# Optimization experiments

Hardware: AMD Instinct MI355X
Metric: run time of the kernel (lower is better)

Reference implementation:

```python
import jax, jax.numpy as jnp
import numpy as np

B, S, DM, NH, WIN = 2, 2048, 1024, 16, 256
DH = DM // NH          # 64
DFF = 4 * DM           # 4096
WIDTHS = (256, 512, 1024)  # 1024 == hidden -> identity (no adapter in torch ModuleDict)


def _ln(x, g, b, eps=1e-5):
    m = jnp.mean(x, -1, keepdims=True)
    v = jnp.var(x, -1, keepdims=True)
    return (x - m) * jax.lax.rsqrt(v + eps) * g + b


def _gelu(t):
    return jax.nn.gelu(t, approximate=False)  # torch nn.GELU default = exact erf


def setup_inputs() -> dict:
    key = jax.random.key(0)
    ks = iter(jax.random.split(key, 32))

    def lin(fi, fo):
        # xavier_uniform(gain=1/sqrt(2)) ~ scale sqrt(2/(fi+fo))/sqrt(2); normal init is fine for a numeric reference
        std = float((1.0 / np.sqrt(2.0)) * np.sqrt(2.0 / (fi + fo)))
        return (jax.random.normal(next(ks), (fi, fo), jnp.float32) * std,
                jnp.zeros((fo,), jnp.float32))

    inp = {}
    inp['x'] = jax.random.normal(next(ks), (B, S, DM), jnp.float32)
    inp['width_multiplier'] = jax.random.uniform(next(ks), (B, S, 1), jnp.float32)
    # attention projections
    inp['wq'], inp['bq'] = lin(DM, DM)
    inp['wk'], inp['bk'] = lin(DM, DM)
    inp['wv'], inp['bv'] = lin(DM, DM)
    inp['wo'], inp['bo'] = lin(DM, DM)
    inp['lnq_g'] = jnp.ones((DH,), jnp.float32); inp['lnq_b'] = jnp.zeros((DH,), jnp.float32)
    inp['lnk_g'] = jnp.ones((DH,), jnp.float32); inp['lnk_b'] = jnp.zeros((DH,), jnp.float32)
    # base FFN
    inp['fc1_w'], inp['fc1_b'] = lin(DM, DFF)
    inp['fc2_w'], inp['fc2_b'] = lin(DFF, DM)
    inp['lni_g'] = jnp.ones((DM,), jnp.float32); inp['lni_b'] = jnp.zeros((DM,), jnp.float32)
    inp['lnh_g'] = jnp.ones((DFF,), jnp.float32); inp['lnh_b'] = jnp.zeros((DFF,), jnp.float32)
    # width adapters (for widths != hidden_dim)
    inp['a256_w1'], inp['a256_b1'] = lin(DM, 256)
    inp['a256_w2'], inp['a256_b2'] = lin(256, DM)
    inp['a512_w1'], inp['a512_b1'] = lin(DM, 512)
    inp['a512_w2'], inp['a512_b2'] = lin(512, DM)
    # router output: index into WIDTHS per token
    inp['width_idx'] = jax.random.randint(next(ks), (B, S), 0, 3)
    return inp


def reference(x, width_multiplier, wq, bq, wk, bk, wv, bv, wo, bo,
              lnq_g, lnq_b, lnk_g, lnk_b, fc1_w, fc1_b, fc2_w, fc2_b,
              lni_g, lni_b, lnh_g, lnh_b,
              a256_w1, a256_b1, a256_w2, a256_b2,
              a512_w1, a512_b1, a512_w2, a512_b2, width_idx):
    # ---- local causal windowed attention pathway ----
    q = (x @ wq + bq).reshape(B, S, NH, DH)
    k = (x @ wk + bk).reshape(B, S, NH, DH)
    v = (x @ wv + bv).reshape(B, S, NH, DH)
    q = _ln(q, lnq_g, lnq_b)  # per-head-dim LayerNorm (torch ln_q on [B,S,H,Dh])
    k = _ln(k, lnk_g, lnk_b)
    scores = jnp.einsum('bihd,bjhd->bhij', q, k) / np.float32(np.sqrt(DH))
    ii = jnp.arange(S)[:, None]
    jj = jnp.arange(S)[None, :]
    allowed = (jj <= ii) & (ii - jj <= WIN)  # causal + local window
    scores = jnp.where(allowed[None, None], scores, -jnp.inf)
    probs = jax.nn.softmax(scores, axis=-1)
    attn = jnp.einsum('bhij,bjhd->bihd', probs, v).reshape(B, S, DM)
    h = x + attn @ wo + bo  # residual around attention pathway

    # ---- width-adaptive FFN ----
    xn = _ln(h, lni_g, lni_b)
    hid = _ln(_gelu(xn @ fc1_w + fc1_b), lnh_g, lnh_b)
    base = hid @ fc2_w + fc2_b
    # per-width adapters, combined by routing mask (dense compute, masked scatter)
    a0 = _gelu(xn @ a256_w1 + a256_b1) @ a256_w2 + a256_b2
    a1 = _gelu(xn @ a512_w1 + a512_b1) @ a512_w2 + a512_b2
    a2 = xn  # width == hidden_dim -> identity pass-through
    m0 = (width_idx == 0)[..., None]
    m1 = (width_idx == 1)[..., None]
    m2 = (width_idx == 2)[..., None]
    adaptive = jnp.where(m0, a0, 0.0) + jnp.where(m1, a1, 0.0) + jnp.where(m2, a2, 0.0)
    ffn_out = base * width_multiplier + adaptive * (1.0 - width_multiplier)
    return h + ffn_out
```

## Files before the change

### kernel.cpp

```cpp
#include <hip/hip_runtime.h>
#include <math.h>

#define B_   2
#define S_   2048
#define DM_  1024
#define NH_  16
#define DH_  64
#define DFF_ 4096
#define WIN_ 256
#define MTOK (B_*S_)

typedef unsigned short ushort_t;
typedef short s16x8 __attribute__((ext_vector_type(8)));
typedef float f32x4 __attribute__((ext_vector_type(4)));

__device__ __forceinline__ float b2f(ushort_t u) {
    union { unsigned int i; float f; } c; c.i = ((unsigned int)u) << 16; return c.f;
}
__device__ __forceinline__ ushort_t f2b(float f) {
    union { float f; unsigned int i; } c; c.f = f;
    unsigned int r = c.i + 0x7fffu + ((c.i >> 16) & 1u);
    return (ushort_t)(r >> 16);
}
__device__ __forceinline__ float gelu_fast(float x) {
    const float u = 0.7978845608f * x * fmaf(0.044715f, x * x, 1.0f);
    const float e = __expf(2.0f * u);
    const float t = 1.0f - 2.0f / (e + 1.0f);
    return 0.5f * x * (1.0f + t);
}
__device__ __forceinline__ void gload16(const void* g, void* l) {
    __builtin_amdgcn_global_load_lds(
        (const __attribute__((address_space(1))) unsigned int*)g,
        (__attribute__((address_space(3))) unsigned int*)l, 16, 0, 0);
}
__device__ __forceinline__ int xcd_swz(int wgid, int nwg) {
    const int nx = 8;
    const int q = nwg / nx, r = nwg % nx;
    const int xcd = wgid % nx, lo = wgid / nx;
    const int base = (xcd < r) ? xcd * (q + 1) : r * (q + 1) + (xcd - r) * q;
    return base + lo;
}

__device__ __forceinline__ void gemm_loop(
    const ushort_t* __restrict__ A, int lda,
    const ushort_t* __restrict__ Bt, int ldb,
    int Kc, int bx, int by, f32x4 (&acc)[4][4])
{
    __shared__ __align__(16) ushort_t As[256 * 64];
    __shared__ __align__(16) ushort_t Bs[128 * 64];

    const int tid  = threadIdx.x;
    const int lane = tid & 63;
    const int w    = tid >> 6;
    const int row0 = by * 256;
    const int col0 = bx * 128;

    const int srow = lane >> 3;
    const int sk   = (lane & 7) * 8;
    const int wr   = (w >> 1) * 64;
    const int wc   = (w & 1) * 64;
    const int lr   = lane & 15;
    const int lk   = (lane >> 4) * 8;

    for (int k0 = 0; k0 < Kc; k0 += 64) {
        #pragma unroll
        for (int i = 0; i < 4; ++i) {
            const int c = i * 8 + w;
            const int cr = c * 8 + srow;
            gload16(A + (size_t)(row0 + cr) * lda + k0 + sk, (char*)As + c * 1024);
        }
        #pragma unroll
        for (int i = 0; i < 2; ++i) {
            const int c = i * 8 + w;
            const int cr = c * 8 + srow;
            gload16(Bt + (size_t)(col0 + cr) * ldb + k0 + sk, (char*)Bs + c * 1024);
        }
        __syncthreads();
        #pragma unroll
        for (int ks = 0; ks < 2; ++ks) {
            s16x8 af[4], bfr[4];
            #pragma unroll
            for (int mi = 0; mi < 4; ++mi)
                af[mi] = *(const s16x8*)&As[(wr + mi * 16 + lr) * 64 + ks * 32 + lk];
            #pragma unroll
            for (int ni = 0; ni < 4; ++ni)
                bfr[ni] = *(const s16x8*)&Bs[(wc + ni * 16 + lr) * 64 + ks * 32 + lk];
            #pragma unroll
            for (int mi = 0; mi < 4; ++mi)
                #pragma unroll
                for (int ni = 0; ni < 4; ++ni)
                    acc[mi][ni] = __builtin_amdgcn_mfma_f32_16x16x32_bf16(
                        af[mi], bfr[ni], acc[mi][ni], 0, 0, 0);
        }
        __syncthreads();
    }
}

__global__ __launch_bounds__(512) void gemm_qkvln(
    const ushort_t* __restrict__ A, const ushort_t* __restrict__ Bt,
    const float* __restrict__ bias,
    const float* __restrict__ qg, const float* __restrict__ qb,
    const float* __restrict__ kg, const float* __restrict__ kb,
    ushort_t* __restrict__ qh, ushort_t* __restrict__ kh, ushort_t* __restrict__ vh)
{
    f32x4 acc[4][4] = {};
    gemm_loop(A, 1024, Bt, 1024, 1024, blockIdx.x, blockIdx.y, acc);

    const int lane = threadIdx.x & 63;
    const int w    = threadIdx.x >> 6;
    const int wr   = (w >> 1) * 64;
    const int wc   = (w & 1) * 64;
    const int row0 = blockIdx.y * 256;
    const int col0 = blockIdx.x * 128;
    const int crow = (lane >> 4) * 4;
    const int ccol = lane & 15;
    const int sel  = (col0 + wc) >> 10;
    const int hh   = ((col0 + wc) & 1023) >> 6;
    ushort_t* dst = (sel == 0) ? qh : (sel == 1) ? kh : vh;

    #pragma unroll
    for (int mi = 0; mi < 4; ++mi) {
        float val[4][4];
        float s1[4] = {}, sq[4] = {};
        #pragma unroll
        for (int ni = 0; ni < 4; ++ni) {
            const float bc = bias[col0 + wc + ni * 16 + ccol];
            #pragma unroll
            for (int r = 0; r < 4; ++r) {
                const float v = acc[mi][ni][r] + bc;
                val[ni][r] = v;
                s1[r] += v;
                sq[r] = fmaf(v, v, sq[r]);
            }
        }
        if (sel < 2) {
            #pragma unroll
            for (int r = 0; r < 4; ++r) {
                #pragma unroll
                for (int m = 1; m < 16; m <<= 1) {
                    s1[r] += __shfl_xor(s1[r], m);
                    sq[r] += __shfl_xor(sq[r], m);
                }
            }
        }
        #pragma unroll
        for (int r = 0; r < 4; ++r) {
            const int r_abs = row0 + wr + mi * 16 + crow + r;
            const int bb = r_abs >> 11, ss = r_abs & 2047;
            const size_t db = (((size_t)(bb * NH_ + hh)) * S_ + ss) * 64;
            const float mean = s1[r] * 0.015625f;
            const float var  = sq[r] * 0.015625f - mean * mean;
            const float rstd = rsqrtf(var + 1e-5f);
            #pragma unroll
            for (int ni = 0; ni < 4; ++ni) {
                const int d = ni * 16 + ccol;
                float v = val[ni][r];
                if (sel == 0)      v = ((v - mean) * rstd * qg[d] + qb[d]) * 0.125f;
                else if (sel == 1) v = (v - mean) * rstd * kg[d] + kb[d];
                dst[db + d] = f2b(v);
            }
        }
    }
}

__global__ __launch_bounds__(512) void gemm_fc1ad(
    const ushort_t* __restrict__ A, const ushort_t* __restrict__ Bt,
    const float* __restrict__ bias,
    ushort_t* __restrict__ hid, ushort_t* __restrict__ tA)
{
    f32x4 acc[4][4] = {};
    gemm_loop(A, 1024, Bt, 1024, 1024, blockIdx.x, blockIdx.y, acc);

    const int lane = threadIdx.x & 63;
    const int w    = threadIdx.x >> 6;
    const int wr   = (w >> 1) * 64;
    const int wc   = (w & 1) * 64;
    const int row0 = blockIdx.y * 256;
    const int col0 = blockIdx.x * 128;
    const int crow = (lane >> 4) * 4;
    const int ccol = lane & 15;
    const bool isad = (col0 >= 4096);
    ushort_t* D = isad ? tA : hid;
    const int stride = isad ? 768 : 4096;
    const int cb     = isad ? 4096 : 0;

    #pragma unroll
    for (int ni = 0; ni < 4; ++ni) {
        const int col = col0 + wc + ni * 16 + ccol;
        const float bc = bias[col];
        #pragma unroll
        for (int mi = 0; mi < 4; ++mi) {
            #pragma unroll
            for (int r = 0; r < 4; ++r) {
                const int row = row0 + wr + mi * 16 + crow + r;
                D[(size_t)row * stride + (col - cb)] = f2b(gelu_fast(acc[mi][ni][r] + bc));
            }
        }
    }
}

__device__ __forceinline__ void epi_raw(
    f32x4 (&acc)[4][4], float* __restrict__ C, int N, int bx, int by)
{
    const int lane = threadIdx.x & 63;
    const int w    = threadIdx.x >> 6;
    const int wr   = (w >> 1) * 64;
    const int wc   = (w & 1) * 64;
    const int crow = (lane >> 4) * 4;
    const int ccol = lane & 15;
    #pragma unroll
    for (int ni = 0; ni < 4; ++ni) {
        const int col = bx * 128 + wc + ni * 16 + ccol;
        #pragma unroll
        for (int mi = 0; mi < 4; ++mi) {
            #pragma unroll
            for (int r = 0; r < 4; ++r) {
                const int row = by * 256 + wr + mi * 16 + crow + r;
                C[(size_t)row * N + col] = acc[mi][ni][r];
            }
        }
    }
}

__global__ __launch_bounds__(512) void gemm_wo_sk(
    const ushort_t* __restrict__ A, const ushort_t* __restrict__ Wt,
    float* __restrict__ p0, float* __restrict__ p1)
{
    const int z = blockIdx.z;
    f32x4 acc[4][4] = {};
    gemm_loop(A + z * 512, 1024, Wt + z * 512, 1024, 512, blockIdx.x, blockIdx.y, acc);
    epi_raw(acc, z ? p1 : p0, 1024, blockIdx.x, blockIdx.y);
}

__global__ __launch_bounds__(512) void gemm_fc2_sk(
    const ushort_t* __restrict__ A, const ushort_t* __restrict__ Bt,
    float* __restrict__ p0, float* __restrict__ p1)
{
    const int z = blockIdx.z;
    f32x4 acc[4][4] = {};
    gemm_loop(A + z * 2048, 4096, Bt + z * 2048, 4096, 2048, blockIdx.x, blockIdx.y, acc);
    epi_raw(acc, z ? p1 : p0, 1024, blockIdx.x, blockIdx.y);
}

__global__ __launch_bounds__(512) void gemm_adapters(
    const ushort_t* __restrict__ tA, const ushort_t* __restrict__ w2a,
    const ushort_t* __restrict__ w2b, const float* __restrict__ b2a,
    const float* __restrict__ b2b, float* __restrict__ a0, float* __restrict__ a1)
{
    const int z = blockIdx.z;
    const ushort_t* Ap = z ? tA + 256 : tA;
    const ushort_t* Wp = z ? w2b : w2a;
    const float*    bp = z ? b2b : b2a;
    float*          Cp = z ? a1 : a0;
    const int Kz = z ? 512 : 256;
    f32x4 acc[4][4] = {};
    gemm_loop(Ap, 768, Wp, Kz, Kz, blockIdx.x, blockIdx.y, acc);

    const int lane = threadIdx.x & 63;
    const int w    = threadIdx.x >> 6;
    const int wr   = (w >> 1) * 64;
    const int wc   = (w & 1) * 64;
    const int crow = (lane >> 4) * 4;
    const int ccol = lane & 15;
    #pragma unroll
    for (int ni = 0; ni < 4; ++ni) {
        const int col = blockIdx.x * 128 + wc + ni * 16 + ccol;
        const float bc = bp[col];
        #pragma unroll
        for (int mi = 0; mi < 4; ++mi) {
            #pragma unroll
            for (int r = 0; r < 4; ++r) {
                const int row = blockIdx.y * 256 + wr + mi * 16 + crow + r;
                Cp[(size_t)row * 1024 + col] = acc[mi][ni][r] + bc;
            }
        }
    }
}

__device__ __forceinline__ void wtrans_core(
    const float* __restrict__ W, ushort_t* __restrict__ Wt, int K, int N,
    int bx, int by)
{
    __shared__ float tile[32][33];
    const int n0 = bx * 32, k0 = by * 32;
    const int tx = threadIdx.x & 31, ty = threadIdx.x >> 5;
    #pragma unroll
    for (int j = 0; j < 4; ++j)
        tile[ty + j * 8][tx] = W[(size_t)(k0 + ty + j * 8) * N + n0 + tx];
    __syncthreads();
    #pragma unroll
    for (int j = 0; j < 4; ++j)
        Wt[(size_t)(n0 + ty + j * 8) * K + k0 + tx] = f2b(tile[tx][ty + j * 8]);
}

__global__ __launch_bounds__(256) void wtrans(
    const float* __restrict__ W, ushort_t* __restrict__ Wt, int K, int N)
{
    wtrans_core(W, Wt, K, N, blockIdx.x, blockIdx.y);
}

__global__ __launch_bounds__(256) void wtrans4(
    const float* w0, const float* w1, const float* w2, const float* w3,
    ushort_t* d0, ushort_t* d1, ushort_t* d2, ushort_t* d3)
{
    const int z = blockIdx.z;
    const float* W = (z == 0) ? w0 : (z == 1) ? w1 : (z == 2) ? w2 : w3;
    ushort_t* Wt   = (z == 0) ? d0 : (z == 1) ? d1 : (z == 2) ? d2 : d3;
    wtrans_core(W, Wt, 1024, 1024, blockIdx.x, blockIdx.y);
}

__global__ __launch_bounds__(256) void conv_f2b(
    const float* __restrict__ in, ushort_t* __restrict__ out, int n4)
{
    const int i = blockIdx.x * 256 + threadIdx.x;
    if (i >= n4) return;
    float4 v = ((const float4*)in)[i];
    ushort4 o; o.x = f2b(v.x); o.y = f2b(v.y); o.z = f2b(v.z); o.w = f2b(v.w);
    ((ushort4*)out)[i] = o;
}

__global__ __launch_bounds__(256) void prep_bias(
    const float* bq, const float* bk, const float* bv, const float* fb,
    const float* b1, const float* b2, float* bqkv, float* bfc1ad)
{
    const int t = blockIdx.x * 256 + threadIdx.x;
    if (t < 1024) { bqkv[t] = bq[t]; bqkv[1024 + t] = bk[t]; bqkv[2048 + t] = bv[t]; }
    if (t < 4096)      bfc1ad[t] = fb[t];
    else if (t < 4352) bfc1ad[t] = b1[t - 4096];
    else if (t < 4864) bfc1ad[t] = b2[t - 4352];
}

__global__ __launch_bounds__(256) void attn_mfma(
    const ushort_t* __restrict__ qh, const ushort_t* __restrict__ kh,
    const ushort_t* __restrict__ vh, ushort_t* __restrict__ o)
{
    __shared__ __align__(16) ushort_t Ks[64 * 64];
    __shared__ __align__(16) ushort_t Vt[64 * 64];
    __shared__ __align__(16) ushort_t Pl[4 * 16 * 64];

    const int bid = xcd_swz(blockIdx.x, gridDim.x);
    const int qt  = bid & 31;
    const int hh  = (bid >> 5) & 15;
    const int b   = bid >> 9;
    const int wq   = threadIdx.x >> 6;
    const int lane = threadIdx.x & 63;
    const int lg  = lane >> 4;
    const int lq  = lane & 15;

    const int i0  = qt * 64;
    const int iw0 = i0 + wq * 16;
    const int i_l = iw0 + lq;

    const size_t plane = ((size_t)(b * NH_ + hh)) * S_ * 64;

    s16x8 qf[2];
    {
        const ushort_t* qp = qh + plane + (size_t)(iw0 + lq) * 64 + lg * 8;
        qf[0] = *(const s16x8*)(qp);
        qf[1] = *(const s16x8*)(qp + 32);
    }

    f32x4 acc[4] = {};
    float M = -1e30f, L = 0.0f;

    const int jstart = (i0 - WIN_) > 0 ? (i0 - WIN_) : 0;
    const int nt     = (i0 + 64 - jstart) >> 6;

    const int srow0 = threadIdx.x >> 3;
    const int sd0   = (threadIdx.x & 7) * 8;

    for (int t = 0; t < nt; ++t) {
        const int j0 = jstart + t * 64;

        #pragma unroll
        for (int pass = 0; pass < 2; ++pass) {
            const int skey = srow0 + pass * 32;
            const size_t src = plane + (size_t)(j0 + skey) * 64 + sd0;
            s16x8 k8 = *(const s16x8*)(kh + src);
            s16x8 v8 = *(const s16x8*)(vh + src);
            *(s16x8*)&Ks[skey * 64 + (sd0 ^ ((skey & 7) << 3))] = k8;
            #pragma unroll
            for (int e = 0; e < 8; ++e) {
                const int d = sd0 + e;
                Vt[d * 64 + (skey ^ (((d >> 1) & 7) << 3))] = (ushort_t)v8[e];
            }
        }
        __syncthreads();

        f32x4 sc[4];
        #pragma unroll
        for (int kt = 0; kt < 4; ++kt) {
            const int krow = kt * 16 + lq;
            const int swk = (krow & 7) << 3;
            s16x8 k0 = *(const s16x8*)&Ks[krow * 64 + ((lg * 8) ^ swk)];
            s16x8 k1 = *(const s16x8*)&Ks[krow * 64 + ((lg * 8 + 32) ^ swk)];
            f32x4 z = {};
            z = __builtin_amdgcn_mfma_f32_16x16x32_bf16(k0, qf[0], z, 0, 0, 0);
            z = __builtin_amdgcn_mfma_f32_16x16x32_bf16(k1, qf[1], z, 0, 0, 0);
            sc[kt] = z;
        }

        const bool fullv = (j0 + 63 <= iw0) && (iw0 + 15 - j0 <= WIN_);
        if (!fullv) {
            #pragma unroll
            for (int kt = 0; kt < 4; ++kt)
                #pragma unroll
                for (int r = 0; r < 4; ++r) {
                    const int jv = j0 + kt * 16 + lg * 4 + r;
                    const int dd = i_l - jv;
                    const bool ok = (dd >= 0) && (dd <= WIN_);
                    sc[kt][r] = ok ? sc[kt][r] : -1e30f;
                }
        }
        float mx = -1e30f;
        #pragma unroll
        for (int kt = 0; kt < 4; ++kt)
            #pragma unroll
            for (int r = 0; r < 4; ++r) mx = fmaxf(mx, sc[kt][r]);
        mx = fmaxf(mx, __shfl_xor(mx, 16));
        mx = fmaxf(mx, __shfl_xor(mx, 32));
        const float nM = fmaxf(M, mx);
        const float alpha = __expf(M - nM);
        M = nM;
        float ts = 0.0f;
        float ev[16];
        #pragma unroll
        for (int kt = 0; kt < 4; ++kt)
            #pragma unroll
            for (int r = 0; r < 4; ++r) {
                float e = __expf(sc[kt][r] - nM);
                if (!fullv) e = (sc[kt][r] > -1e29f) ? e : 0.0f;
                ev[kt * 4 + r] = e;
                ts += e;
            }
        ts += __shfl_xor(ts, 16);
        ts += __shfl_xor(ts, 32);
        L = L * alpha + ts;

        {
            ushort_t* pw = Pl + wq * 1024;
            const int swq = (lq & 7) << 3;
            #pragma unroll
            for (int kt = 0; kt < 4; ++kt)
                #pragma unroll
                for (int pr = 0; pr < 2; ++pr) {
                    const int key0 = kt * 16 + lg * 4 + pr * 2;
                    const unsigned int pk =
                        (unsigned int)f2b(ev[kt * 4 + pr * 2]) |
                        ((unsigned int)f2b(ev[kt * 4 + pr * 2 + 1]) << 16);
                    *(unsigned int*)&pw[lq * 64 + (key0 ^ swq)] = pk;
                }
        }

        float ar[4];
        #pragma unroll
        for (int r = 0; r < 4; ++r) ar[r] = __shfl(alpha, lg * 4 + r);
        #pragma unroll
        for (int dt = 0; dt < 4; ++dt)
            #pragma unroll
            for (int r = 0; r < 4; ++r) acc[dt][r] *= ar[r];

        {
            const ushort_t* pw = Pl + wq * 1024;
            const int swq = (lq & 7) << 3;
            s16x8 pf0 = *(const s16x8*)&pw[lq * 64 + ((lg * 8) ^ swq)];
            s16x8 pf1 = *(const s16x8*)&pw[lq * 64 + ((lg * 8 + 32) ^ swq)];
            #pragma unroll
            for (int dt = 0; dt < 4; ++dt) {
                const int d = dt * 16 + lq;
                const int swd = ((d >> 1) & 7) << 3;
                s16x8 v0 = *(const s16x8*)&Vt[d * 64 + ((lg * 8) ^ swd)];
                s16x8 v1 = *(const s16x8*)&Vt[d * 64 + ((lg * 8 + 32) ^ swd)];
                acc[dt] = __builtin_amdgcn_mfma_f32_16x16x32_bf16(pf0, v0, acc[dt], 0, 0, 0);
                acc[dt] = __builtin_amdgcn_mfma_f32_16x16x32_bf16(pf1, v1, acc[dt], 0, 0, 0);
            }
        }
        __syncthreads();
    }

    const float inv = 1.0f / L;
    float ir[4];
    #pragma unroll
    for (int r = 0; r < 4; ++r) ir[r] = __shfl(inv, lg * 4 + r);
    #pragma unroll
    for (int dt = 0; dt < 4; ++dt)
        #pragma unroll
        for (int r = 0; r < 4; ++r) {
            const int qq = lg * 4 + r;
            o[((size_t)(b * S_ + iw0 + qq)) * DM_ + hh * 64 + dt * 16 + lq] =
                f2b(acc[dt][r] * ir[r]);
        }
}

__global__ __launch_bounds__(256) void ln_token_h(
    const float* __restrict__ p0, const float* __restrict__ p1,
    const float* __restrict__ bo, const float* __restrict__ x,
    float* __restrict__ hb, ushort_t* __restrict__ xnb,
    const float* __restrict__ g, const float* __restrict__ b)
{
    const int t = blockIdx.x;
    const size_t base = (size_t)t * 1024;
    float vals[4];
    float s = 0.0f, s2 = 0.0f;
    #pragma unroll
    for (int i = 0; i < 4; ++i) {
        const int idx = i * 256 + threadIdx.x;
        const float v = x[base + idx] + p0[base + idx] + p1[base + idx] + bo[idx];
        hb[base + idx] = v;
        vals[i] = v;
        s += v;
        s2 = fmaf(v, v, s2);
    }
    #pragma unroll
    for (int o = 32; o >= 1; o >>= 1) { s += __shfl_xor(s, o); s2 += __shfl_xor(s2, o); }
    __shared__ float rs[4], rq[4];
    const int wid = threadIdx.x >> 6, lane = threadIdx.x & 63;
    if (lane == 0) { rs[wid] = s; rq[wid] = s2; }
    __syncthreads();
    s  = rs[0] + rs[1] + rs[2] + rs[3];
    s2 = rq[0] + rq[1] + rq[2] + rq[3];
    const float mean = s * (1.0f / 1024.0f);
    const float var  = s2 * (1.0f / 1024.0f) - mean * mean;
    const float rstd = rsqrtf(var + 1e-5f);
    #pragma unroll
    for (int i = 0; i < 4; ++i) {
        const int idx = i * 256 + threadIdx.x;
        xnb[base + idx] = f2b((vals[i] - mean) * rstd * g[idx] + b[idx]);
    }
}

template <int N>
__global__ __launch_bounds__(256) void ln_token2(
    const ushort_t* __restrict__ in, ushort_t* __restrict__ outp,
    const float* __restrict__ g, const float* __restrict__ b)
{
    constexpr int NPT = N / 256;
    const int t = blockIdx.x;
    const ushort_t* row = in + (size_t)t * N;
    float vals[NPT];
    float s = 0.0f, s2 = 0.0f;
    #pragma unroll
    for (int i = 0; i < NPT; ++i) {
        float x = b2f(row[i * 256 + threadIdx.x]);
        vals[i] = x;
        s += x;
        s2 = fmaf(x, x, s2);
    }
    #pragma unroll
    for (int o = 32; o >= 1; o >>= 1) { s += __shfl_xor(s, o); s2 += __shfl_xor(s2, o); }
    __shared__ float rs[4], rq[4];
    const int wid = threadIdx.x >> 6, lane = threadIdx.x & 63;
    if (lane == 0) { rs[wid] = s; rq[wid] = s2; }
    __syncthreads();
    s  = rs[0] + rs[1] + rs[2] + rs[3];
    s2 = rq[0] + rq[1] + rq[2] + rq[3];
    const float mean = s * (1.0f / N);
    const float var  = s2 * (1.0f / N) - mean * mean;
    const float rstd = rsqrtf(var + 1e-5f);
    #pragma unroll
    for (int i = 0; i < NPT; ++i) {
        const int idx = i * 256 + threadIdx.x;
        outp[(size_t)t * N + idx] = f2b((vals[i] - mean) * rstd * g[idx] + b[idx]);
    }
}

__global__ __launch_bounds__(256) void combine3(
    float* __restrict__ outp, const float* __restrict__ p1,
    const float* __restrict__ fc2b, const float* __restrict__ h,
    const ushort_t* __restrict__ xnb, const float* __restrict__ a0,
    const float* __restrict__ a1, const float* __restrict__ wm,
    const int* __restrict__ widx)
{
    const size_t idx = (size_t)blockIdx.x * 256 + threadIdx.x;
    const int t   = (int)(idx >> 10);
    const int col = (int)(idx & 1023);
    const float w = wm[t];
    const int sel = widx[t];
    const float base = outp[idx] + p1[idx] + fc2b[col];
    const float ad = (sel == 0) ? a0[idx] : ((sel == 1) ? a1[idx] : b2f(xnb[idx]));
    outp[idx] = h[idx] + base * w + ad * (1.0f - w);
}

extern "C" void kernel_launch(void* const* d_in, const int* in_sizes, int n_in,
                              void* d_out, int out_size, void* d_ws, size_t ws_size,
                              hipStream_t stream)
{
    const float* x     = (const float*)d_in[0];
    const float* wm    = (const float*)d_in[1];
    const float* wq    = (const float*)d_in[2];
    const float* bq    = (const float*)d_in[3];
    const float* wk    = (const float*)d_in[4];
    const float* bk    = (const float*)d_in[5];
    const float* wv    = (const float*)d_in[6];
    const float* bv    = (const float*)d_in[7];
    const float* wo    = (const float*)d_in[8];
    const float* bo    = (const float*)d_in[9];
    const float* lnq_g = (const float*)d_in[10];
    const float* lnq_b = (const float*)d_in[11];
    const float* lnk_g = (const float*)d_in[12];
    const float* lnk_b = (const float*)d_in[13];
    const float* fc1_w = (const float*)d_in[14];
    const float* fc1_b = (const float*)d_in[15];
    const float* fc2_w = (const float*)d_in[16];
    const float* fc2_b = (const float*)d_in[17];
    const float* lni_g = (const float*)d_in[18];
    const float* lni_b = (const float*)d_in[19];
    const float* lnh_g = (const float*)d_in[20];
    const float* lnh_b = (const float*)d_in[21];
    const float* a256_w1 = (const float*)d_in[22];
    const float* a256_b1 = (const float*)d_in[23];
    const float* a256_w2 = (const float*)d_in[24];
    const float* a256_b2 = (const float*)d_in[25];
    const float* a512_w1 = (const float*)d_in[26];
    const float* a512_b1 = (const float*)d_in[27];
    const float* a512_w2 = (const float*)d_in[28];
    const float* a512_b2 = (const float*)d_in[29];
    const int*   widx    = (const int*)d_in[30];

    float* out = (float*)d_out;

    char* p = (char*)d_ws;
    auto alloc = [&](size_t bytes) { char* r = p; p += (bytes + 255) & ~(size_t)255; return r; };
    float*    ascr  = (float*)   alloc((size_t)MTOK * 2048 * 4);
    float*    hb    = (float*)   alloc((size_t)MTOK * 1024 * 4);
    ushort_t* xnb   = (ushort_t*)alloc((size_t)MTOK * 1024 * 2);
    ushort_t* hidb  = (ushort_t*)alloc((size_t)MTOK * 4096 * 2);
    ushort_t* tA    = (ushort_t*)alloc((size_t)MTOK * 768 * 2);
    ushort_t* WqkvT = (ushort_t*)alloc((size_t)3072 * 1024 * 2);
    ushort_t* WoT   = (ushort_t*)alloc((size_t)1024 * 1024 * 2);
    ushort_t* fc1adT= (ushort_t*)alloc((size_t)4864 * 1024 * 2);
    ushort_t* fc2T  = (ushort_t*)alloc((size_t)1024 * 4096 * 2);
    ushort_t* w2aT  = (ushort_t*)alloc((size_t)1024 * 256 * 2);
    ushort_t* w2bT  = (ushort_t*)alloc((size_t)1024 * 512 * 2);
    float*    bqkv  = (float*)   alloc(3072 * 4);
    float*    bfc1ad= (float*)   alloc(4864 * 4);
    float*    p1    = (float*)   alloc((size_t)MTOK * 1024 * 4);
    ushort_t* xb    = hidb;
    ushort_t* attnb = hidb + (size_t)MTOK * 1024;
    ushort_t* qh    = hidb + (size_t)MTOK * 2048;
    ushort_t* kh    = hidb + (size_t)MTOK * 3072;
    ushort_t* vh    = (ushort_t*)p1;
    float*    a0    = ascr;
    float*    a1    = ascr + (size_t)MTOK * 1024;

    const dim3 blk(256);
    const dim3 blk512(512);

    prep_bias<<<20, blk, 0, stream>>>(bq, bk, bv, fc1_b, a256_b1, a512_b1,
                                      bqkv, bfc1ad);
    conv_f2b<<<(MTOK * 1024 / 4 + 255) / 256, blk, 0, stream>>>(x, xb, MTOK * 1024 / 4);
    wtrans4<<<dim3(32, 32, 4), blk, 0, stream>>>(wq, wk, wv, wo,
        WqkvT, WqkvT + 1024 * 1024, WqkvT + 2048 * 1024, WoT);
    wtrans<<<dim3(128, 32), blk, 0, stream>>>(fc1_w, fc1adT, 1024, 4096);
    wtrans<<<dim3(8, 32),   blk, 0, stream>>>(a256_w1, fc1adT + (size_t)4096 * 1024, 1024, 256);
    wtrans<<<dim3(16, 32),  blk, 0, stream>>>(a512_w1, fc1adT + (size_t)4352 * 1024, 1024, 512);
    wtrans<<<dim3(32, 128), blk, 0, stream>>>(fc2_w, fc2T, 4096, 1024);
    wtrans<<<dim3(32, 8),   blk, 0, stream>>>(a256_w2, w2aT, 256, 1024);
    wtrans<<<dim3(32, 16),  blk, 0, stream>>>(a512_w2, w2bT, 512, 1024);

    gemm_qkvln<<<dim3(24, 16), blk512, 0, stream>>>(xb, WqkvT, bqkv,
        lnq_g, lnq_b, lnk_g, lnk_b, qh, kh, vh);
    attn_mfma<<<B_ * NH_ * (S_ / 64), blk, 0, stream>>>(qh, kh, vh, attnb);

    gemm_wo_sk<<<dim3(8, 16, 2), blk512, 0, stream>>>(attnb, WoT, hb, p1);
    ln_token_h<<<MTOK, blk, 0, stream>>>(hb, p1, bo, x, hb, xnb, lni_g, lni_b);

    gemm_fc1ad<<<dim3(38, 16), blk512, 0, stream>>>(xnb, fc1adT, bfc1ad, hidb, tA);
    ln_token2<DFF_><<<MTOK, blk, 0, stream>>>(hidb, hidb, lnh_g, lnh_b);
    gemm_fc2_sk<<<dim3(8, 16, 2), blk512, 0, stream>>>(hidb, fc2T, out, p1);

    gemm_adapters<<<dim3(8, 16, 2), blk512, 0, stream>>>(tA, w2aT, w2bT,
                                                         a256_b2, a512_b2, a0, a1);

    combine3<<<(int)((size_t)MTOK * 1024 / 256), blk, 0, stream>>>(
        out, p1, fc2_b, hb, xnb, a0, a1, wm, widx);
}
```

Baseline: 346.3 us.

## Double-buffer GEMM shared tiles with K-step 32 to overlap loads and MFMA

Result: faster. 320.2 us (-7.5%).

```diff
diff --git a/kernel.cpp b/kernel.cpp
--- a/kernel.cpp
+++ b/kernel.cpp
@@ -46,8 +46,8 @@
     const ushort_t* __restrict__ Bt, int ldb,
     int Kc, int bx, int by, f32x4 (&acc)[4][4])
 {
-    __shared__ __align__(16) ushort_t As[256 * 64];
-    __shared__ __align__(16) ushort_t Bs[128 * 64];
+    __shared__ __align__(16) ushort_t As[2][256 * 32];
+    __shared__ __align__(16) ushort_t Bs[2][128 * 32];
 
     const int tid  = threadIdx.x;
     const int lane = tid & 63;
@@ -55,44 +55,49 @@
     const int row0 = by * 256;
     const int col0 = bx * 128;
 
-    const int srow = lane >> 3;
-    const int sk   = (lane & 7) * 8;
+    const int srow = lane >> 2;
+    const int sk   = (lane & 3) * 8;
     const int wr   = (w >> 1) * 64;
     const int wc   = (w & 1) * 64;
     const int lr   = lane & 15;
     const int lk   = (lane >> 4) * 8;
 
-    for (int k0 = 0; k0 < Kc; k0 += 64) {
-        #pragma unroll
-        for (int i = 0; i < 4; ++i) {
-            const int c = i * 8 + w;
-            const int cr = c * 8 + srow;
-            gload16(A + (size_t)(row0 + cr) * lda + k0 + sk, (char*)As + c * 1024);
-        }
+    auto stage = [&](int buf, int k0) {
         #pragma unroll
         for (int i = 0; i < 2; ++i) {
             const int c = i * 8 + w;
-            const int cr = c * 8 + srow;
-            gload16(Bt + (size_t)(col0 + cr) * ldb + k0 + sk, (char*)Bs + c * 1024);
-        }
+            const int cr = c * 16 + srow;
+            gload16(A + (size_t)(row0 + cr) * lda + k0 + sk,
+                    (char*)As[buf] + c * 1024);
+        }
+        {
+            const int cr = w * 16 + srow;
+            gload16(Bt + (size_t)(col0 + cr) * ldb + k0 + sk,
+                    (char*)Bs[buf] + w * 1024);
+        }
+    };
+
+    const int nk = Kc >> 5;
+    stage(0, 0);
+    __syncthreads();
+    int cur = 0;
+    for (int k = 0; k < nk; ++k) {
+        if (k + 1 < nk) stage(cur ^ 1, (k + 1) << 5);
+        s16x8 af[4], bfr[4];
+        #pragma unroll
+        for (int mi = 0; mi < 4; ++mi)
+            af[mi] = *(const s16x8*)&As[cur][(wr + mi * 16 + lr) * 32 + lk];
+        #pragma unroll
+        for (int ni = 0; ni < 4; ++ni)
+            bfr[ni] = *(const s16x8*)&Bs[cur][(wc + ni * 16 + lr) * 32 + lk];
+        #pragma unroll
+        for (int mi = 0; mi < 4; ++mi)
+            #pragma unroll
+            for (int ni = 0; ni < 4; ++ni)
+                acc[mi][ni] = __builtin_amdgcn_mfma_f32_16x16x32_bf16(
+                    af[mi], bfr[ni], acc[mi][ni], 0, 0, 0);
         __syncthreads();
-        #pragma unroll
-        for (int ks = 0; ks < 2; ++ks) {
-            s16x8 af[4], bfr[4];
-            #pragma unroll
-            for (int mi = 0; mi < 4; ++mi)
-                af[mi] = *(const s16x8*)&As[(wr + mi * 16 + lr) * 64 + ks * 32 + lk];
-            #pragma unroll
-            for (int ni = 0; ni < 4; ++ni)
-                bfr[ni] = *(const s16x8*)&Bs[(wc + ni * 16 + lr) * 64 + ks * 32 + lk];
-            #pragma unroll
-            for (int mi = 0; mi < 4; ++mi)
-                #pragma unroll
-                for (int ni = 0; ni < 4; ++ni)
-                    acc[mi][ni] = __builtin_amdgcn_mfma_f32_16x16x32_bf16(
-                        af[mi], bfr[ni], acc[mi][ni], 0, 0, 0);
-        }
-        __syncthreads();
+        cur ^= 1;
     }
 }
 
```
